# Kernel tuning notes

Measured on AMD Instinct MI355X. Metric: run time of the kernel, lower is better.

The kernel has to match this reference:

```python
import jax, jax.numpy as jnp
import numpy as np


def setup_inputs() -> dict:
    key = jax.random.key(0)
    kq, kk, kv = jax.random.split(key, 3)
    B, L, Q, H, E = 8, 128, 8, 8, 64
    S, P = 128, 8
    queries = jax.random.normal(kq, (B, L, Q, H, E), dtype=jnp.float32)
    keys = jax.random.normal(kk, (B, S, P, H, E), dtype=jnp.float32)
    values = jax.random.normal(kv, (B, S, P, H, E), dtype=jnp.float32)
    attn_mask = jnp.zeros((1,), dtype=bool)  # unused by the module
    return {"queries": queries, "keys": keys, "values": values, "attn_mask": attn_mask}


def reference(queries, keys, values, attn_mask):
    # queries: [B,L,Q,H,E]; keys/values: [B,S,P,H,E]
    B, L, Q, H, E = queries.shape
    S, P = values.shape[1], values.shape[2]
    scale = 1.0 / np.sqrt(E).astype(np.float32)
    # scores: [B,S,P,L,Q,H]
    scores = jnp.einsum('blqhe,bsphe->bsplqh', queries, keys)
    # softmax over joint (S,P) axis
    scaled = (scale * scores).reshape(B, S * P, L, Q, H)
    attn = jax.nn.softmax(scaled, axis=1).reshape(B, S, P, L, Q, H)
    # dropout is identity in eval / with p=0.0
    V = jnp.einsum('bsphe,bsplqh->blqhe', values, attn)
    return V
```

## Files before the change

### kernel.cpp

```cpp
#include <hip/hip_runtime.h>
#include <hip/hip_bf16.h>

typedef __attribute__((ext_vector_type(4))) float f32x4;
typedef __attribute__((ext_vector_type(16))) float f32x16;
typedef __attribute__((ext_vector_type(8))) short bf16x8;
typedef __attribute__((ext_vector_type(4))) unsigned u32x4;

#define MFMA32(a, b, c) __builtin_amdgcn_mfma_f32_32x32x16_bf16(a, b, c, 0, 0, 0)
#define EXP2(x) __builtin_amdgcn_exp2f(x)

constexpr int NQ = 1024;
constexpr int NK = 1024;
constexpr int RS = 512;
constexpr int Ec = 64;
constexpr int KT = 128;
constexpr int NT = NK / KT;
constexpr float QSCALE2 = 0.125f * 1.4426950408889634f;

__device__ __forceinline__ short f2bf(float x) {
    return (short)__builtin_bit_cast(unsigned short, __float2bfloat16(x));
}

__device__ __forceinline__ bf16x8 pack2(float4 a, float4 b) {
    bf16x8 r;
    r[0] = f2bf(a.x); r[1] = f2bf(a.y); r[2] = f2bf(a.z); r[3] = f2bf(a.w);
    r[4] = f2bf(b.x); r[5] = f2bf(b.y); r[6] = f2bf(b.z); r[7] = f2bf(b.w);
    return r;
}

__device__ __forceinline__ bf16x8 pack2s(float4 a, float4 b, float s) {
    bf16x8 r;
    r[0] = f2bf(a.x * s); r[1] = f2bf(a.y * s); r[2] = f2bf(a.z * s); r[3] = f2bf(a.w * s);
    r[4] = f2bf(b.x * s); r[5] = f2bf(b.y * s); r[6] = f2bf(b.z * s); r[7] = f2bf(b.w * s);
    return r;
}

__device__ __forceinline__ unsigned cvtpk(float a, float b) {
    unsigned lo = (unsigned short)__builtin_bit_cast(unsigned short, __float2bfloat16(a));
    unsigned hi = (unsigned short)__builtin_bit_cast(unsigned short, __float2bfloat16(b));
    return lo | (hi << 16);
}

__device__ __forceinline__ void gload16(const short* src, short* dst) {
    __builtin_amdgcn_global_load_lds((const __attribute__((address_space(1))) void*)src,
                                     (__attribute__((address_space(3))) void*)dst, 16, 0, 0);
}

__global__ __launch_bounds__(256, 4)
void cvt_kv(const float* __restrict__ Kg, const float* __restrict__ Vg,
            short* __restrict__ Kbf, short* __restrict__ Vt) {
    __shared__ __attribute__((aligned(16))) short Vl[64][72];
    const int tid  = threadIdx.x;
    const int head = blockIdx.x >> 4;
    const int kb   = blockIdx.x & 15;
    const int b    = head >> 3, h = head & 7;
    const int row  = tid >> 2, q = tid & 3;

    const size_t gin = (((size_t)(b * NK + kb * 64 + row)) * 8 + h) * 64 + q * 16;
    const float4* kp = (const float4*)(Kg + gin);
    float4 k0 = kp[0], k1 = kp[1], k2 = kp[2], k3 = kp[3];
    short* kout = Kbf + ((size_t)head * NK + kb * 64 + row) * 64 + q * 16;
    ((bf16x8*)kout)[0] = pack2(k0, k1);
    ((bf16x8*)kout)[1] = pack2(k2, k3);

    const float4* vp = (const float4*)(Vg + gin);
    float4 v0 = vp[0], v1 = vp[1], v2 = vp[2], v3 = vp[3];
    const float vv[16] = {v0.x, v0.y, v0.z, v0.w, v1.x, v1.y, v1.z, v1.w,
                          v2.x, v2.y, v2.z, v2.w, v3.x, v3.y, v3.z, v3.w};
#pragma unroll
    for (int j = 0; j < 16; ++j) Vl[q * 16 + j][row] = f2bf(vv[j]);
    __syncthreads();
    short* vout = Vt + ((size_t)head * Ec + row) * NK + kb * 64 + q * 16;
    ((bf16x8*)vout)[0] = *(const bf16x8*)&Vl[row][q * 16];
    ((bf16x8*)vout)[1] = *(const bf16x8*)&Vl[row][q * 16 + 8];
}

__global__ __launch_bounds__(256, 2)
void fully_attn_kernel(const float* __restrict__ Qg, const short* __restrict__ Kbf,
                       const short* __restrict__ Vt, float* __restrict__ Og) {
    __shared__ __attribute__((aligned(16))) short Kl[2][KT][64];
    __shared__ __attribute__((aligned(16))) short Vl[64][KT];

    const int tid  = threadIdx.x;
    const int lane = tid & 63;
    const int wv   = tid >> 6;
    const int ql   = lane & 31;
    const int hi   = lane >> 5;
    const int swz  = (lane & 7) << 4;

    const int bid  = blockIdx.x;
    const int head = (bid & 7) * 8 + (bid >> 6);
    const int qb   = (bid >> 3) & 7;
    const int b    = head >> 3, h = head & 7;

    const size_t headQ = (size_t)b * NQ * RS + (size_t)h * Ec;
    const short* Kh = Kbf + (size_t)head * NK * Ec;
    const short* Vh = Vt + (size_t)head * Ec * NK;

    const int qrow = qb * 128 + wv * 32 + ql;
    const float* qp = Qg + headQ + (size_t)qrow * RS;
    bf16x8 qf[4];
#pragma unroll
    for (int j = 0; j < 4; ++j) {
        const float4* q4 = (const float4*)(qp + j * 16 + hi * 8);
        qf[j] = pack2s(q4[0], q4[1], QSCALE2);
    }

    const int klocal = lane >> 3;
    const int kj     = (lane & 7) ^ (klocal & 7);
    const int vlocal = lane >> 4;

#define STAGE_K(buf, tt)                                                          \
    {                                                                             \
        _Pragma("unroll")                                                         \
        for (int s = 0; s < 4; ++s)                                               \
            gload16(Kh + (size_t)((tt) * KT + wv * 32 + s * 8 + klocal) * 64 +    \
                        kj * 8,                                                   \
                    &Kl[buf][wv * 32 + s * 8][0]);                                \
    }

#define STAGE_V(tt)                                                               \
    {                                                                             \
        _Pragma("unroll")                                                         \
        for (int s = 0; s < 4; ++s)                                               \
            gload16(Vh + (size_t)(wv * 16 + s * 4 + vlocal) * NK + (tt) * KT +    \
                        (((lane & 15) ^ ((s * 4 + vlocal) & 7)) * 8),             \
                    &Vl[wv * 16 + s * 4][0]);                                     \
    }

    STAGE_K(0, 0);
    STAGE_V(0);

    float l_r = 0.0f;
    f32x16 o0 = (f32x16)(0.0f), o1 = (f32x16)(0.0f);

    int cur = 0;
    for (int t = 0; t < NT; ++t) {
        __syncthreads();

        bf16x8 kf[4][4];
#pragma unroll
        for (int kt = 0; kt < 4; ++kt) {
            const char* kr = (const char*)&Kl[cur][kt * 32 + ql][0];
#pragma unroll
            for (int j = 0; j < 4; ++j)
                kf[kt][j] = *(const bf16x8*)(kr + ((j * 32 + hi * 16) ^ swz));
        }
        f32x16 p[4];
        __builtin_amdgcn_s_setprio(1);
#pragma unroll
        for (int kt = 0; kt < 4; ++kt) {
            f32x16 acc = (f32x16)(0.0f);
#pragma unroll
            for (int j = 0; j < 4; ++j) acc = MFMA32(kf[kt][j], qf[j], acc);
            p[kt] = acc;
        }
        __builtin_amdgcn_s_setprio(0);

        bf16x8 vf0[8], vf1[8];
#pragma unroll
        for (int m = 0; m < 8; ++m) {
            const int cb = (m * 32 + hi * 16) ^ swz;
            vf0[m] = *(const bf16x8*)((const char*)&Vl[ql][0] + cb);
            vf1[m] = *(const bf16x8*)((const char*)&Vl[32 + ql][0] + cb);
        }

        __syncthreads();
        if (t + 1 < NT) {
            STAGE_V(t + 1);
            STAGE_K(cur ^ 1, t + 1);
        }

        float rs0 = 0.f, rs1 = 0.f, rs2 = 0.f, rs3 = 0.f;
#pragma unroll
        for (int kt = 0; kt < 4; ++kt)
#pragma unroll
            for (int i = 0; i < 16; i += 4) {
                float e0 = EXP2(p[kt][i + 0]);
                float e1 = EXP2(p[kt][i + 1]);
                float e2 = EXP2(p[kt][i + 2]);
                float e3 = EXP2(p[kt][i + 3]);
                p[kt][i + 0] = e0; p[kt][i + 1] = e1;
                p[kt][i + 2] = e2; p[kt][i + 3] = e3;
                rs0 += e0; rs1 += e1; rs2 += e2; rs3 += e3;
            }
        l_r += (rs0 + rs1) + (rs2 + rs3);

        __builtin_amdgcn_s_setprio(1);
#pragma unroll
        for (int m = 0; m < 8; ++m) {
            const int kt = m >> 1, r0 = (m & 1) * 8;
            unsigned a0 = cvtpk(p[kt][r0 + 0], p[kt][r0 + 1]);
            unsigned a1 = cvtpk(p[kt][r0 + 2], p[kt][r0 + 3]);
            unsigned b0 = cvtpk(p[kt][r0 + 4], p[kt][r0 + 5]);
            unsigned b1 = cvtpk(p[kt][r0 + 6], p[kt][r0 + 7]);
            asm("v_permlane32_swap_b32 %0, %1" : "+v"(a0), "+v"(b0));
            asm("v_permlane32_swap_b32 %0, %1" : "+v"(a1), "+v"(b1));
            u32x4 w = {a0, a1, b0, b1};
            bf16x8 pf = __builtin_bit_cast(bf16x8, w);
            o0 = MFMA32(vf0[m], pf, o0);
            o1 = MFMA32(vf1[m], pf, o1);
        }
        __builtin_amdgcn_s_setprio(0);

        cur ^= 1;
    }

    l_r += __shfl_xor(l_r, 32);
    const float inv = 1.0f / l_r;
    float* op = Og + headQ + (size_t)qrow * RS;
#pragma unroll
    for (int bnk = 0; bnk < 4; ++bnk) {
        float4 s0 = {o0[bnk * 4 + 0] * inv, o0[bnk * 4 + 1] * inv,
                     o0[bnk * 4 + 2] * inv, o0[bnk * 4 + 3] * inv};
        float4 s1 = {o1[bnk * 4 + 0] * inv, o1[bnk * 4 + 1] * inv,
                     o1[bnk * 4 + 2] * inv, o1[bnk * 4 + 3] * inv};
        *(float4*)(op + bnk * 8 + hi * 4)      = s0;
        *(float4*)(op + 32 + bnk * 8 + hi * 4) = s1;
    }
}

extern "C" void kernel_launch(void* const* d_in, const int* in_sizes, int n_in,
                              void* d_out, int out_size, void* d_ws, size_t ws_size,
                              hipStream_t stream) {
    const float* Qg = (const float*)d_in[0];
    const float* Kg = (const float*)d_in[1];
    const float* Vg = (const float*)d_in[2];
    float* Og = (float*)d_out;

    short* Kbf = (short*)d_ws;
    short* Vt  = (short*)d_ws + (size_t)64 * NK * Ec;

    hipLaunchKernelGGL(cvt_kv, dim3(64 * 16), dim3(256), 0, stream, Kg, Vg, Kbf, Vt);
    hipLaunchKernelGGL(fully_attn_kernel, dim3(512), dim3(256), 0, stream,
                       Qg, Kbf, Vt, Og);
}
```

Before: 41.50 us.

## Split key tiles across two wave groups per block and double-buffer V

Each block now runs 8 waves instead of 4. Two groups of waves share the same query rows, and each group handles half of every 128-key tile. Their partial outputs and row sums are combined through shared memory at the end. V staging is now double-buffered like K, and the loads for the next tile are issued at the top of each iteration with a single barrier per iteration. This aims for more waves in flight and more latency hiding, at the cost of a cross-group reduction, doubled V shared memory, and lower register headroom from launch_bounds(512,4).

```diff
diff --git a/kernel.cpp b/kernel.cpp
--- a/kernel.cpp
+++ b/kernel.cpp
@@ -75,15 +75,17 @@
     ((bf16x8*)vout)[1] = *(const bf16x8*)&Vl[row][q * 16 + 8];
 }
 
-__global__ __launch_bounds__(256, 2)
+__global__ __launch_bounds__(512, 4)
 void fully_attn_kernel(const float* __restrict__ Qg, const short* __restrict__ Kbf,
                        const short* __restrict__ Vt, float* __restrict__ Og) {
     __shared__ __attribute__((aligned(16))) short Kl[2][KT][64];
-    __shared__ __attribute__((aligned(16))) short Vl[64][KT];
+    __shared__ __attribute__((aligned(16))) short Vl[2][64][KT];
 
     const int tid  = threadIdx.x;
     const int lane = tid & 63;
     const int wv   = tid >> 6;
+    const int grp  = wv & 3;
+    const int par  = wv >> 2;
     const int ql   = lane & 31;
     const int hi   = lane >> 5;
     const int swz  = (lane & 7) << 4;
@@ -97,7 +99,7 @@
     const short* Kh = Kbf + (size_t)head * NK * Ec;
     const short* Vh = Vt + (size_t)head * Ec * NK;
 
-    const int qrow = qb * 128 + wv * 32 + ql;
+    const int qrow = qb * 128 + grp * 32 + ql;
     const float* qp = Qg + headQ + (size_t)qrow * RS;
     bf16x8 qf[4];
 #pragma unroll
@@ -106,74 +108,59 @@
         qf[j] = pack2s(q4[0], q4[1], QSCALE2);
     }
 
-    const int klocal = lane >> 3;
-    const int kj     = (lane & 7) ^ (klocal & 7);
-    const int vlocal = lane >> 4;
+    const int krow8 = lane >> 3;
+    const int kj    = (lane & 7) ^ krow8;
+    const int vrow4 = lane >> 4;
 
 #define STAGE_K(buf, tt)                                                          \
     {                                                                             \
         _Pragma("unroll")                                                         \
-        for (int s = 0; s < 4; ++s)                                               \
-            gload16(Kh + (size_t)((tt) * KT + wv * 32 + s * 8 + klocal) * 64 +    \
+        for (int s = 0; s < 2; ++s)                                               \
+            gload16(Kh + (size_t)((tt) * KT + wv * 16 + s * 8 + krow8) * 64 +     \
                         kj * 8,                                                   \
-                    &Kl[buf][wv * 32 + s * 8][0]);                                \
-    }
-
-#define STAGE_V(tt)                                                               \
+                    &Kl[buf][wv * 16 + s * 8][0]);                                \
+    }
+
+#define STAGE_V(buf, tt)                                                          \
     {                                                                             \
         _Pragma("unroll")                                                         \
-        for (int s = 0; s < 4; ++s)                                               \
-            gload16(Vh + (size_t)(wv * 16 + s * 4 + vlocal) * NK + (tt) * KT +    \
-                        (((lane & 15) ^ ((s * 4 + vlocal) & 7)) * 8),             \
-                    &Vl[wv * 16 + s * 4][0]);                                     \
+        for (int s = 0; s < 2; ++s)                                               \
+            gload16(Vh + (size_t)(wv * 8 + s * 4 + vrow4) * NK + (tt) * KT +      \
+                        (((lane & 15) ^ ((s * 4 + vrow4) & 7)) * 8),              \
+                    &Vl[buf][wv * 8 + s * 4][0]);                                 \
     }
 
     STAGE_K(0, 0);
-    STAGE_V(0);
+    STAGE_V(0, 0);
+    __syncthreads();
 
     float l_r = 0.0f;
     f32x16 o0 = (f32x16)(0.0f), o1 = (f32x16)(0.0f);
 
     int cur = 0;
     for (int t = 0; t < NT; ++t) {
-        __syncthreads();
-
-        bf16x8 kf[4][4];
-#pragma unroll
-        for (int kt = 0; kt < 4; ++kt) {
-            const char* kr = (const char*)&Kl[cur][kt * 32 + ql][0];
-#pragma unroll
-            for (int j = 0; j < 4; ++j)
-                kf[kt][j] = *(const bf16x8*)(kr + ((j * 32 + hi * 16) ^ swz));
-        }
-        f32x16 p[4];
-        __builtin_amdgcn_s_setprio(1);
-#pragma unroll
-        for (int kt = 0; kt < 4; ++kt) {
-            f32x16 acc = (f32x16)(0.0f);
-#pragma unroll
-            for (int j = 0; j < 4; ++j) acc = MFMA32(kf[kt][j], qf[j], acc);
+        if (t + 1 < NT) { STAGE_K(cur ^ 1, t + 1); STAGE_V(cur ^ 1, t + 1); }
+
+        f32x16 p[2];
+#pragma unroll
+        for (int kt = 0; kt < 2; ++kt) {
+            const char* kr = (const char*)&Kl[cur][par * 64 + kt * 32 + ql][0];
+            bf16x8 kf0 = *(const bf16x8*)(kr + ((0 * 32 + hi * 16) ^ swz));
+            bf16x8 kf1 = *(const bf16x8*)(kr + ((1 * 32 + hi * 16) ^ swz));
+            bf16x8 kf2 = *(const bf16x8*)(kr + ((2 * 32 + hi * 16) ^ swz));
+            bf16x8 kf3 = *(const bf16x8*)(kr + ((3 * 32 + hi * 16) ^ swz));
+            __builtin_amdgcn_s_setprio(1);
+            f32x16 acc = MFMA32(kf0, qf[0], (f32x16)(0.0f));
+            acc = MFMA32(kf1, qf[1], acc);
+            acc = MFMA32(kf2, qf[2], acc);
+            acc = MFMA32(kf3, qf[3], acc);
+            __builtin_amdgcn_s_setprio(0);
             p[kt] = acc;
         }
-        __builtin_amdgcn_s_setprio(0);
-
-        bf16x8 vf0[8], vf1[8];
-#pragma unroll
-        for (int m = 0; m < 8; ++m) {
-            const int cb = (m * 32 + hi * 16) ^ swz;
-            vf0[m] = *(const bf16x8*)((const char*)&Vl[ql][0] + cb);
-            vf1[m] = *(const bf16x8*)((const char*)&Vl[32 + ql][0] + cb);
-        }
-
-        __syncthreads();
-        if (t + 1 < NT) {
-            STAGE_V(t + 1);
-            STAGE_K(cur ^ 1, t + 1);
-        }
 
         float rs0 = 0.f, rs1 = 0.f, rs2 = 0.f, rs3 = 0.f;
 #pragma unroll
-        for (int kt = 0; kt < 4; ++kt)
+        for (int kt = 0; kt < 2; ++kt)
 #pragma unroll
             for (int i = 0; i < 16; i += 4) {
                 float e0 = EXP2(p[kt][i + 0]);
@@ -186,9 +173,11 @@
             }
         l_r += (rs0 + rs1) + (rs2 + rs3);
 
+        const char* vr0 = (const char*)&Vl[cur][ql][0];
+        const char* vr1 = (const char*)&Vl[cur][32 + ql][0];
         __builtin_amdgcn_s_setprio(1);
 #pragma unroll
-        for (int m = 0; m < 8; ++m) {
+        for (int m = 0; m < 4; ++m) {
             const int kt = m >> 1, r0 = (m & 1) * 8;
             unsigned a0 = cvtpk(p[kt][r0 + 0], p[kt][r0 + 1]);
             unsigned a1 = cvtpk(p[kt][r0 + 2], p[kt][r0 + 3]);
@@ -198,25 +187,47 @@
             asm("v_permlane32_swap_b32 %0, %1" : "+v"(a1), "+v"(b1));
             u32x4 w = {a0, a1, b0, b1};
             bf16x8 pf = __builtin_bit_cast(bf16x8, w);
-            o0 = MFMA32(vf0[m], pf, o0);
-            o1 = MFMA32(vf1[m], pf, o1);
+            const int cb = (par * 128 + m * 32 + hi * 16) ^ swz;
+            bf16x8 v0 = *(const bf16x8*)(vr0 + cb);
+            bf16x8 v1 = *(const bf16x8*)(vr1 + cb);
+            o0 = MFMA32(v0, pf, o0);
+            o1 = MFMA32(v1, pf, o1);
         }
         __builtin_amdgcn_s_setprio(0);
 
+        __syncthreads();
         cur ^= 1;
     }
 
     l_r += __shfl_xor(l_r, 32);
-    const float inv = 1.0f / l_r;
-    float* op = Og + headQ + (size_t)qrow * RS;
-#pragma unroll
-    for (int bnk = 0; bnk < 4; ++bnk) {
-        float4 s0 = {o0[bnk * 4 + 0] * inv, o0[bnk * 4 + 1] * inv,
-                     o0[bnk * 4 + 2] * inv, o0[bnk * 4 + 3] * inv};
-        float4 s1 = {o1[bnk * 4 + 0] * inv, o1[bnk * 4 + 1] * inv,
-                     o1[bnk * 4 + 2] * inv, o1[bnk * 4 + 3] * inv};
-        *(float4*)(op + bnk * 8 + hi * 4)      = s0;
-        *(float4*)(op + 32 + bnk * 8 + hi * 4) = s1;
+
+    float* scrO = (float*)&Kl[0][0][0];
+    float* scrL = (float*)&Vl[0][0][0];
+    const int slot = grp * 64 + lane;
+    if (par == 1) {
+#pragma unroll
+        for (int i = 0; i < 16; ++i) {
+            scrO[i * 256 + slot]        = o0[i];
+            scrO[(16 + i) * 256 + slot] = o1[i];
+        }
+        scrL[slot] = l_r;
+    }
+    __syncthreads();
+    if (par == 0) {
+        const float inv = 1.0f / (l_r + scrL[slot]);
+        float* op = Og + headQ + (size_t)qrow * RS;
+#pragma unroll
+        for (int bnk = 0; bnk < 4; ++bnk) {
+            float4 s0, s1;
+#pragma unroll
+            for (int j = 0; j < 4; ++j) {
+                const int i = bnk * 4 + j;
+                ((float*)&s0)[j] = (o0[i] + scrO[i * 256 + slot]) * inv;
+                ((float*)&s1)[j] = (o1[i] + scrO[(16 + i) * 256 + slot]) * inv;
+            }
+            *(float4*)(op + bnk * 8 + hi * 4)      = s0;
+            *(float4*)(op + 32 + bnk * 8 + hi * 4) = s1;
+        }
     }
 }
 
@@ -232,6 +243,6 @@
     short* Vt  = (short*)d_ws + (size_t)64 * NK * Ec;
 
     hipLaunchKernelGGL(cvt_kv, dim3(64 * 16), dim3(256), 0, stream, Kg, Vg, Kbf, Vt);
-    hipLaunchKernelGGL(fully_attn_kernel, dim3(512), dim3(256), 0, stream,
+    hipLaunchKernelGGL(fully_attn_kernel, dim3(512), dim3(512), 0, stream,
                        Qg, Kbf, Vt, Og);
 }
```

New measurement: 43.71 us. +5.3%, slower.

## Software-pipeline QK^T of next tile with PV of previous tile

Applied to the files above, without the earlier changes.

Restructures the main loop so each iteration computes QK^T for tile t and PV for tile t-1 while exp/pack results are carried in registers across iterations. V gets a triple-buffered LDS ring and K and V are prefetched two tiles ahead, so MFMA work can overlap the exp stage and the global loads. This raises register pressure (pfv plus p live across iterations) and LDS use, which may reduce occupancy at the 2-blocks-per-CU launch bound.

```diff
diff --git a/kernel.cpp b/kernel.cpp
--- a/kernel.cpp
+++ b/kernel.cpp
@@ -79,7 +79,7 @@
 void fully_attn_kernel(const float* __restrict__ Qg, const short* __restrict__ Kbf,
                        const short* __restrict__ Vt, float* __restrict__ Og) {
     __shared__ __attribute__((aligned(16))) short Kl[2][KT][64];
-    __shared__ __attribute__((aligned(16))) short Vl[64][KT];
+    __shared__ __attribute__((aligned(16))) short Vl[3][64][KT];
 
     const int tid  = threadIdx.x;
     const int lane = tid & 63;
@@ -119,92 +119,111 @@
                     &Kl[buf][wv * 32 + s * 8][0]);                                \
     }
 
-#define STAGE_V(tt)                                                               \
+#define STAGE_V(slot, tt)                                                         \
     {                                                                             \
         _Pragma("unroll")                                                         \
         for (int s = 0; s < 4; ++s)                                               \
             gload16(Vh + (size_t)(wv * 16 + s * 4 + vlocal) * NK + (tt) * KT +    \
                         (((lane & 15) ^ ((s * 4 + vlocal) & 7)) * 8),             \
-                    &Vl[wv * 16 + s * 4][0]);                                     \
+                    &Vl[slot][wv * 16 + s * 4][0]);                               \
+    }
+
+#define QKT(buf)                                                                  \
+    {                                                                             \
+        bf16x8 kf[4][4];                                                          \
+        _Pragma("unroll")                                                         \
+        for (int kt = 0; kt < 4; ++kt) {                                          \
+            const char* kr = (const char*)&Kl[buf][kt * 32 + ql][0];              \
+            _Pragma("unroll")                                                     \
+            for (int j = 0; j < 4; ++j)                                           \
+                kf[kt][j] = *(const bf16x8*)(kr + ((j * 32 + hi * 16) ^ swz));    \
+        }                                                                         \
+        __builtin_amdgcn_s_setprio(1);                                            \
+        _Pragma("unroll")                                                         \
+        for (int kt = 0; kt < 4; ++kt) {                                          \
+            f32x16 acc = (f32x16)(0.0f);                                          \
+            _Pragma("unroll")                                                     \
+            for (int j = 0; j < 4; ++j) acc = MFMA32(kf[kt][j], qf[j], acc);      \
+            p[kt] = acc;                                                          \
+        }                                                                         \
+        __builtin_amdgcn_s_setprio(0);                                            \
+    }
+
+#define PV(slot)                                                                  \
+    {                                                                             \
+        bf16x8 vf0[8], vf1[8];                                                    \
+        _Pragma("unroll")                                                         \
+        for (int m = 0; m < 8; ++m) {                                             \
+            const int cb = (m * 32 + hi * 16) ^ swz;                              \
+            vf0[m] = *(const bf16x8*)((const char*)&Vl[slot][ql][0] + cb);        \
+            vf1[m] = *(const bf16x8*)((const char*)&Vl[slot][32 + ql][0] + cb);   \
+        }                                                                         \
+        __builtin_amdgcn_s_setprio(1);                                            \
+        _Pragma("unroll")                                                         \
+        for (int m = 0; m < 8; ++m) {                                             \
+            bf16x8 pf = __builtin_bit_cast(bf16x8, pfv[m]);                       \
+            o0 = MFMA32(vf0[m], pf, o0);                                          \
+            o1 = MFMA32(vf1[m], pf, o1);                                          \
+        }                                                                         \
+        __builtin_amdgcn_s_setprio(0);                                            \
+    }
+
+#define EXPPACK()                                                                 \
+    {                                                                             \
+        float rs0 = 0.f, rs1 = 0.f, rs2 = 0.f, rs3 = 0.f;                         \
+        _Pragma("unroll")                                                         \
+        for (int kt = 0; kt < 4; ++kt)                                            \
+            _Pragma("unroll")                                                     \
+            for (int i = 0; i < 16; i += 4) {                                     \
+                float e0 = EXP2(p[kt][i + 0]);                                    \
+                float e1 = EXP2(p[kt][i + 1]);                                    \
+                float e2 = EXP2(p[kt][i + 2]);                                    \
+                float e3 = EXP2(p[kt][i + 3]);                                    \
+                p[kt][i + 0] = e0; p[kt][i + 1] = e1;                             \
+                p[kt][i + 2] = e2; p[kt][i + 3] = e3;                             \
+                rs0 += e0; rs1 += e1; rs2 += e2; rs3 += e3;                       \
+            }                                                                     \
+        l_r += (rs0 + rs1) + (rs2 + rs3);                                         \
+        _Pragma("unroll")                                                         \
+        for (int m = 0; m < 8; ++m) {                                             \
+            const int kt = m >> 1, r0 = (m & 1) * 8;                              \
+            unsigned a0 = cvtpk(p[kt][r0 + 0], p[kt][r0 + 1]);                    \
+            unsigned a1 = cvtpk(p[kt][r0 + 2], p[kt][r0 + 3]);                    \
+            unsigned b0 = cvtpk(p[kt][r0 + 4], p[kt][r0 + 5]);                    \
+            unsigned b1 = cvtpk(p[kt][r0 + 6], p[kt][r0 + 7]);                    \
+            asm("v_permlane32_swap_b32 %0, %1" : "+v"(a0), "+v"(b0));             \
+            asm("v_permlane32_swap_b32 %0, %1" : "+v"(a1), "+v"(b1));             \
+            pfv[m] = (u32x4){a0, a1, b0, b1};                                     \
+        }                                                                         \
     }
 
     STAGE_K(0, 0);
-    STAGE_V(0);
+    STAGE_V(0, 0);
+    __syncthreads();
+    STAGE_K(1, 1);
+    STAGE_V(1, 1);
 
     float l_r = 0.0f;
     f32x16 o0 = (f32x16)(0.0f), o1 = (f32x16)(0.0f);
-
-    int cur = 0;
-    for (int t = 0; t < NT; ++t) {
-        __syncthreads();
-
-        bf16x8 kf[4][4];
-#pragma unroll
-        for (int kt = 0; kt < 4; ++kt) {
-            const char* kr = (const char*)&Kl[cur][kt * 32 + ql][0];
-#pragma unroll
-            for (int j = 0; j < 4; ++j)
-                kf[kt][j] = *(const bf16x8*)(kr + ((j * 32 + hi * 16) ^ swz));
-        }
-        f32x16 p[4];
-        __builtin_amdgcn_s_setprio(1);
-#pragma unroll
-        for (int kt = 0; kt < 4; ++kt) {
-            f32x16 acc = (f32x16)(0.0f);
-#pragma unroll
-            for (int j = 0; j < 4; ++j) acc = MFMA32(kf[kt][j], qf[j], acc);
-            p[kt] = acc;
-        }
-        __builtin_amdgcn_s_setprio(0);
-
-        bf16x8 vf0[8], vf1[8];
-#pragma unroll
-        for (int m = 0; m < 8; ++m) {
-            const int cb = (m * 32 + hi * 16) ^ swz;
-            vf0[m] = *(const bf16x8*)((const char*)&Vl[ql][0] + cb);
-            vf1[m] = *(const bf16x8*)((const char*)&Vl[32 + ql][0] + cb);
-        }
-
+    f32x16 p[4];
+    u32x4 pfv[8];
+
+    QKT(0);
+    EXPPACK();
+
+    for (int t = 1; t < NT; ++t) {
+        const int cur = t & 1;
         __syncthreads();
         if (t + 1 < NT) {
-            STAGE_V(t + 1);
             STAGE_K(cur ^ 1, t + 1);
+            STAGE_V((t + 1) % 3, t + 1);
         }
-
-        float rs0 = 0.f, rs1 = 0.f, rs2 = 0.f, rs3 = 0.f;
-#pragma unroll
-        for (int kt = 0; kt < 4; ++kt)
-#pragma unroll
-            for (int i = 0; i < 16; i += 4) {
-                float e0 = EXP2(p[kt][i + 0]);
-                float e1 = EXP2(p[kt][i + 1]);
-                float e2 = EXP2(p[kt][i + 2]);
-                float e3 = EXP2(p[kt][i + 3]);
-                p[kt][i + 0] = e0; p[kt][i + 1] = e1;
-                p[kt][i + 2] = e2; p[kt][i + 3] = e3;
-                rs0 += e0; rs1 += e1; rs2 += e2; rs3 += e3;
-            }
-        l_r += (rs0 + rs1) + (rs2 + rs3);
-
-        __builtin_amdgcn_s_setprio(1);
-#pragma unroll
-        for (int m = 0; m < 8; ++m) {
-            const int kt = m >> 1, r0 = (m & 1) * 8;
-            unsigned a0 = cvtpk(p[kt][r0 + 0], p[kt][r0 + 1]);
-            unsigned a1 = cvtpk(p[kt][r0 + 2], p[kt][r0 + 3]);
-            unsigned b0 = cvtpk(p[kt][r0 + 4], p[kt][r0 + 5]);
-            unsigned b1 = cvtpk(p[kt][r0 + 6], p[kt][r0 + 7]);
-            asm("v_permlane32_swap_b32 %0, %1" : "+v"(a0), "+v"(b0));
-            asm("v_permlane32_swap_b32 %0, %1" : "+v"(a1), "+v"(b1));
-            u32x4 w = {a0, a1, b0, b1};
-            bf16x8 pf = __builtin_bit_cast(bf16x8, w);
-            o0 = MFMA32(vf0[m], pf, o0);
-            o1 = MFMA32(vf1[m], pf, o1);
-        }
-        __builtin_amdgcn_s_setprio(0);
-
-        cur ^= 1;
-    }
+        QKT(cur);
+        PV((t - 1) % 3);
+        EXPPACK();
+    }
+
+    PV((NT - 1) % 3);
 
     l_r += __shfl_xor(l_r, 32);
     const float inv = 1.0f / l_r;
```

After: 44.01 us. 1.06x slower.
